# Kernel optimization log

Hardware: AMD Instinct MI355X
Metric: run time of the kernel (lower is better)

Reference implementation:

```python
import jax, jax.numpy as jnp
import numpy as np

TONECURVE_LENGTH = 256
RESOLUTION = 1024  # tone_curve_resolution
B, H, W = 8, 1024, 1536

RANGES = {
    'Temperature': (2000.0, 50000.0),
    'Tint': (-150.0, 150.0),
    'Exposure2012': (-5.0, 5.0),
    'Contrast2012': (-100.0, 100.0),
    'Highlights2012': (-100.0, 100.0),
    'Shadows2012': (-100.0, 100.0),
    'Whites2012': (-100.0, 100.0),
    'Blacks2012': (-100.0, 100.0),
    'Vibrance': (-100.0, 100.0),
    'Saturation': (-100.0, 100.0),
}

def _denorm(name, v):
    lo, hi = RANGES[name]
    return lo + 0.5 * (v + 1.0) * (hi - lo)

def _luminance(img):
    return 0.2126 * img[:, 0:1] + 0.7152 * img[:, 1:2] + 0.0722 * img[:, 2:3]

def _white_balance(img, temperature, tint):
    temp = jnp.clip(temperature, 2000.0, 50000.0)
    tr = 6500.0 / temp
    red = jnp.sqrt(tr)
    blue = 1.0 / jnp.sqrt(tr)
    ts = jnp.clip(tint / 150.0, -1.5, 1.5)
    green = 1.0 - 0.1 * ts
    red = red * (1.0 + 0.05 * ts)
    blue = blue * (1.0 - 0.05 * ts)
    gains = jnp.stack([red, green, blue], axis=1)[:, :, None, None]  # [B,3,1,1]
    balanced = img * gains
    norm = jnp.max(gains, axis=1, keepdims=True)
    return jnp.clip(balanced / jnp.maximum(norm, 1e-4), 0.0, 4.0)

def _region(img, luma, value, pivot, width):
    strength = (value / 100.0)[:, None, None, None]
    mask = jax.nn.sigmoid((luma - pivot) / width)
    mask = mask - jnp.mean(mask, axis=(2, 3), keepdims=True)
    new_luma = jnp.clip(luma + strength * mask, 0.0, 1.0)
    ratio = jnp.where(luma > 1e-4, new_luma / jnp.maximum(luma, 1e-4), 1.0)
    return jnp.clip(img * ratio, 0.0, 1.0), new_luma

def _tone_curve(img, tone_curve):
    luma = jnp.clip(_luminance(img), 0.0, 1.0)  # [B,1,H,W]
    # linear interp of [B,L] control points to [B,RESOLUTION], align_corners=True
    src = jnp.arange(RESOLUTION, dtype=jnp.float32) * ((TONECURVE_LENGTH - 1) / (RESOLUTION - 1))
    i0 = jnp.floor(src).astype(jnp.int32)
    i1 = jnp.minimum(i0 + 1, TONECURVE_LENGTH - 1)
    w = src - i0.astype(jnp.float32)
    curve = tone_curve[:, i0] * (1.0 - w) + tone_curve[:, i1] * w  # [B,RESOLUTION]
    coords = luma * (RESOLUTION - 1)
    idx_low = jnp.floor(coords).astype(jnp.int32)
    idx_high = jnp.minimum(idx_low + 1, RESOLUTION - 1)
    weight = coords - idx_low.astype(jnp.float32)
    b = img.shape[0]
    g_low = jnp.take_along_axis(curve, idx_low.reshape(b, -1), axis=1).reshape(luma.shape)
    g_high = jnp.take_along_axis(curve, idx_high.reshape(b, -1), axis=1).reshape(luma.shape)
    target = (1.0 - weight) * g_low + weight * g_high
    ratio = jnp.where(luma > 1e-5, target / jnp.maximum(luma, 1e-5), 1.0)
    return jnp.clip(img * ratio, 0.0, 1.0)

def _vibrance(img, vibrance):
    luma = _luminance(img)
    chroma = img - luma
    cn = jnp.sqrt(jnp.sum(chroma * chroma, axis=1, keepdims=True) + 1e-6)
    mask = jnp.exp(-4.0 * cn)
    gain = jnp.clip(1.0 + (vibrance / 100.0)[:, None, None, None] * mask, 0.2, 4.0)
    return jnp.clip(luma + chroma * gain, 0.0, 1.0)

def _saturation(img, saturation):
    luma = _luminance(img)
    chroma = img - luma
    gain = (1.0 + saturation / 100.0)[:, None, None, None]
    return jnp.clip(luma + chroma * gain, 0.0, 1.0)


def setup_inputs() -> dict:
    key = jax.random.key(0)
    ks = jax.random.split(key, 12)
    sliders = {}
    names = ['temperature_n', 'tint_n', 'exposure_n', 'contrast_n', 'highlights_n',
             'shadows_n', 'whites_n', 'blacks_n', 'vibrance_n', 'saturation_n']
    for i, n in enumerate(names):
        sliders[n] = jax.random.uniform(ks[i], (B,), jnp.float32, -1.0, 1.0)
    image = jax.random.uniform(ks[10], (B, 3, H, W), jnp.float32)
    tone_curve = jnp.sort(jax.random.uniform(ks[11], (B, TONECURVE_LENGTH), jnp.float32), axis=1)
    return {'image': image, 'tone_curve': tone_curve, **sliders}


def reference(image, tone_curve, temperature_n, tint_n, exposure_n, contrast_n,
              highlights_n, shadows_n, whites_n, blacks_n, vibrance_n, saturation_n):
    img = jnp.clip(image, 0.0, 1.0)
    temperature = _denorm('Temperature', temperature_n)
    tint = _denorm('Tint', tint_n)
    exposure = _denorm('Exposure2012', exposure_n)
    contrast = _denorm('Contrast2012', contrast_n)
    highlights = _denorm('Highlights2012', highlights_n)
    shadows = _denorm('Shadows2012', shadows_n)
    whites = _denorm('Whites2012', whites_n)
    blacks = _denorm('Blacks2012', blacks_n)
    vibrance = _denorm('Vibrance', vibrance_n)
    saturation = _denorm('Saturation', saturation_n)

    img = _white_balance(img, temperature, tint)
    img = img * jnp.power(2.0, exposure)[:, None, None, None]  # exposure
    img = jnp.clip(img, 0.0, 4.0)
    factor = (1.0 + contrast / 100.0)[:, None, None, None]      # contrast
    img = jnp.clip((img - 0.5) * factor + 0.5, 0.0, 1.0)

    luma = jnp.clip(_luminance(img), 0.0, 1.0)
    img, luma = _region(img, luma, highlights, 0.7, 0.1)
    img, luma = _region(img, luma, shadows, 0.3, 0.12)
    img, luma = _region(img, luma, whites, 0.9, 0.08)
    img, luma = _region(img, luma, blacks, 0.1, 0.08)

    img = _tone_curve(img, tone_curve)
    img = _vibrance(img, vibrance)
    img = _saturation(img, saturation)
    return jnp.clip(img, 0.0, 1.0)
```

## Files before the change

kernel.cpp:

```cpp
#include <hip/hip_runtime.h>
#include <math.h>

#define H_DIM 1024
#define W_DIM 1536
#define HW_PIX (H_DIM * W_DIM)
#define NBATCH 8
#define QPB (HW_PIX / 4)
#define BLKB 96
#define NBLK (NBATCH * BLKB)
#define QPT (QPB / (BLKB * 256))
#define RESOLUTION 1024
#define TC_LEN 256
#define SPIN_CAP 500000

typedef float vfloat4 __attribute__((ext_vector_type(4)));
typedef unsigned long long u64;

struct Sliders {
    const float* temperature; const float* tint; const float* exposure; const float* contrast;
    const float* highlights;  const float* shadows; const float* whites; const float* blacks;
    const float* vibrance;    const float* saturation;
};

__device__ __forceinline__ float denorm(float v, float lo, float hi) {
    return lo + 0.5f * (v + 1.0f) * (hi - lo);
}
__device__ __forceinline__ float clamp01(float x) {
    return __builtin_amdgcn_fmed3f(x, 0.f, 1.f);
}
__device__ __forceinline__ float clampf(float x, float lo, float hi) {
    return fminf(fmaxf(x, lo), hi);
}
__device__ __forceinline__ float sigmoidf(float x) {
    float t = __builtin_amdgcn_exp2f(x * -1.4426950408889634f);
    return __builtin_amdgcn_rcpf(1.0f + t);
}

struct FrontP { float sr, sg, sb, em, cf; };

__device__ __forceinline__ FrontP front_params(const Sliders& S, int b) {
    float temp = clampf(denorm(S.temperature[b], 2000.f, 50000.f), 2000.f, 50000.f);
    float tr   = 6500.f / temp;
    float red  = sqrtf(tr);
    float blue = 1.0f / sqrtf(tr);
    float ts   = clampf(denorm(S.tint[b], -150.f, 150.f) * (1.0f / 150.0f), -1.5f, 1.5f);
    float green = 1.0f - 0.1f * ts;
    red  *= (1.0f + 0.05f * ts);
    blue *= (1.0f - 0.05f * ts);
    float norm = fmaxf(fmaxf(red, green), blue);
    float inv  = 1.0f / fmaxf(norm, 1e-4f);
    FrontP p;
    p.sr = red * inv; p.sg = green * inv; p.sb = blue * inv;
    p.em = exp2f(denorm(S.exposure[b], -5.f, 5.f));
    p.cf = 1.0f + denorm(S.contrast[b], -100.f, 100.f) * 0.01f;
    return p;
}

__device__ __forceinline__ float front_chan(float x, float s, float em, float cf) {
    x = clamp01(x);
    x = x * s;
    x = fminf(x * em, 4.0f);
    return clamp01((x - 0.5f) * cf + 0.5f);
}

__device__ __forceinline__ float luminance(float r, float g, float b) {
    return 0.2126f * r + 0.7152f * g + 0.0722f * b;
}

__device__ __forceinline__ double block_sum_d(double v) {
    #pragma unroll
    for (int o = 32; o > 0; o >>= 1) v += __shfl_down(v, o, 64);
    __shared__ double s[4];
    int lane = threadIdx.x & 63, wid = threadIdx.x >> 6;
    if (lane == 0) s[wid] = v;
    __syncthreads();
    double r = 0.0;
    if (threadIdx.x == 0) r = s[0] + s[1] + s[2] + s[3];
    return r;
}

__device__ __forceinline__ void build_curve(float* curve, const float* tone_curve, int b) {
    const float* tc = tone_curve + b * TC_LEN;
    for (int j = threadIdx.x; j < RESOLUTION; j += 256) {
        float src = (float)j * ((float)(TC_LEN - 1) / (float)(RESOLUTION - 1));
        float fi  = floorf(src);
        int   i0  = (int)fi;
        int   i1  = min(i0 + 1, TC_LEN - 1);
        float w   = src - fi;
        curve[j]  = tc[i0] * (1.0f - w) + tc[i1] * w;
    }
}

__device__ __forceinline__ float publish_mean(int slot, int b, int bb, double acc,
                                              u64* part, unsigned int* meanc) {
    double tot = block_sum_d(acc);
    __shared__ float msh;
    const int pbase = (slot * NBATCH + b) * BLKB;
    const int tid = threadIdx.x;

    if (bb == 0) {
        double v = 0.0;
        if (tid == 0) v = tot;
        else if (tid < BLKB) {
            u64 x; int spins = 0;
            while ((x = __hip_atomic_load(&part[pbase + tid], __ATOMIC_RELAXED,
                                          __HIP_MEMORY_SCOPE_AGENT)) == 0ull) {
                __builtin_amdgcn_s_sleep(2);
                if (++spins > SPIN_CAP) break;
            }
            v = __builtin_bit_cast(double, x);
        }
        double t2 = block_sum_d(v);
        if (tid == 0) {
            float m = (float)(t2 * (1.0 / (double)HW_PIX));
            msh = m;
            __hip_atomic_store(&meanc[(slot * NBATCH + b) * 16],
                               __builtin_bit_cast(unsigned int, m),
                               __ATOMIC_RELAXED, __HIP_MEMORY_SCOPE_AGENT);
        }
    } else {
        if (tid == 0) {
            __hip_atomic_store(&part[pbase + bb], __builtin_bit_cast(u64, tot),
                               __ATOMIC_RELAXED, __HIP_MEMORY_SCOPE_AGENT);
            unsigned int x; int spins = 0;
            while ((x = __hip_atomic_load(&meanc[(slot * NBATCH + b) * 16],
                                          __ATOMIC_RELAXED,
                                          __HIP_MEMORY_SCOPE_AGENT)) == 0u) {
                __builtin_amdgcn_s_sleep(2);
                if (++spins > SPIN_CAP) break;
            }
            msh = __builtin_bit_cast(float, x);
        }
    }
    __syncthreads();
    float m = msh;
    __syncthreads();
    return m;
}

template <int K>
__device__ __forceinline__ double phaseB_acc(const unsigned short* __restrict__ lslice,
                                             int bb, int tid,
                                             const float* pivots, const float* invw,
                                             const float* strength, const float* meanv) {
    double acc = 0.0;
    for (int it = 0; it < QPT; it++) {
        const int off = (bb * (256 * QPT) + it * 256 + tid) * 4;
        ushort4 lq = *reinterpret_cast<const ushort4*>(lslice + off);
        const unsigned short* qs = reinterpret_cast<const unsigned short*>(&lq);
        #pragma unroll
        for (int i = 0; i < 4; i++) {
            float l = (float)qs[i] * (1.0f / 65535.0f);
            #pragma unroll
            for (int j = 0; j < K; j++) {
                float mask = sigmoidf((l - pivots[j]) * invw[j]);
                l = clamp01(l + strength[j] * (mask - meanv[j]));
            }
            acc += (double)sigmoidf((l - pivots[K]) * invw[K]);
        }
    }
    return acc;
}

__global__ __launch_bounds__(256, 4)
void mega_kernel(const float* __restrict__ image, const float* __restrict__ tone_curve,
                 Sliders S, unsigned int* __restrict__ meanc, u64* __restrict__ part,
                 unsigned short* __restrict__ ws_luma, float* __restrict__ out)
{
    const int b   = blockIdx.x / BLKB;
    const int bb  = blockIdx.x % BLKB;
    const int tid = threadIdx.x;

    __shared__ float curve[RESOLUTION];
    build_curve(curve, tone_curve, b);

    const float pivots[4] = {0.7f, 0.3f, 0.9f, 0.1f};
    const float invw[4]   = {1.0f / 0.1f, 1.0f / 0.12f, 1.0f / 0.08f, 1.0f / 0.08f};
    const float* sliders[4] = {S.highlights, S.shadows, S.whites, S.blacks};

    FrontP p = front_params(S, b);
    float strength[4];
    #pragma unroll
    for (int k = 0; k < 4; k++)
        strength[k] = denorm(sliders[k][b], -100.f, 100.f) * 0.01f;
    float vib  = denorm(S.vibrance[b],   -100.f, 100.f) * 0.01f;
    float satg = 1.0f + denorm(S.saturation[b], -100.f, 100.f) * 0.01f;

    unsigned short* lslice = ws_luma + (size_t)b * HW_PIX;
    const float* ibase = image + (size_t)b * 3 * HW_PIX;

    double acc = 0.0;
    for (int it = 0; it < QPT; it++) {
        const int off = (bb * (256 * QPT) + it * 256 + tid) * 4;
        float4 r4 = *reinterpret_cast<const float4*>(ibase + off);
        float4 g4 = *reinterpret_cast<const float4*>(ibase + HW_PIX + off);
        float4 b4 = *reinterpret_cast<const float4*>(ibase + 2 * HW_PIX + off);
        const float* rr  = reinterpret_cast<const float*>(&r4);
        const float* gg  = reinterpret_cast<const float*>(&g4);
        const float* bb4 = reinterpret_cast<const float*>(&b4);
        ushort4 pk;
        unsigned short* pks = reinterpret_cast<unsigned short*>(&pk);
        #pragma unroll
        for (int i = 0; i < 4; i++) {
            float r  = front_chan(rr[i],  p.sr, p.em, p.cf);
            float g  = front_chan(gg[i],  p.sg, p.em, p.cf);
            float bl = front_chan(bb4[i], p.sb, p.em, p.cf);
            float l  = clamp01(luminance(r, g, bl));
            acc += (double)sigmoidf((l - pivots[0]) * invw[0]);
            pks[i] = (unsigned short)(l * 65535.0f + 0.5f);
        }
        *reinterpret_cast<ushort4*>(lslice + off) = pk;
    }

    float meanv[4];
    meanv[0] = publish_mean(0, b, bb, acc, part, meanc);
    meanv[1] = publish_mean(1, b, bb,
                 phaseB_acc<1>(lslice, bb, tid, pivots, invw, strength, meanv), part, meanc);
    meanv[2] = publish_mean(2, b, bb,
                 phaseB_acc<2>(lslice, bb, tid, pivots, invw, strength, meanv), part, meanc);
    meanv[3] = publish_mean(3, b, bb,
                 phaseB_acc<3>(lslice, bb, tid, pivots, invw, strength, meanv), part, meanc);

    for (int it = 0; it < QPT; it++) {
        const int off = (bb * (256 * QPT) + it * 256 + tid) * 4;
        float4 r4 = *reinterpret_cast<const float4*>(ibase + off);
        float4 g4 = *reinterpret_cast<const float4*>(ibase + HW_PIX + off);
        float4 b4 = *reinterpret_cast<const float4*>(ibase + 2 * HW_PIX + off);
        float* rr  = reinterpret_cast<float*>(&r4);
        float* gg  = reinterpret_cast<float*>(&g4);
        float* bb4 = reinterpret_cast<float*>(&b4);

        #pragma unroll
        for (int i = 0; i < 4; i++) {
            float r  = front_chan(rr[i],  p.sr, p.em, p.cf);
            float g  = front_chan(gg[i],  p.sg, p.em, p.cf);
            float bl = front_chan(bb4[i], p.sb, p.em, p.cf);
            float lum = clamp01(luminance(r, g, bl));

            #pragma unroll
            for (int k = 0; k < 4; k++) {
                float mask = sigmoidf((lum - pivots[k]) * invw[k]);
                float nl   = clamp01(lum + strength[k] * (mask - meanv[k]));
                float ratio = (lum > 1e-4f) ? nl * __builtin_amdgcn_rcpf(lum) : 1.0f;
                r  = fminf(r * ratio, 1.f);
                g  = fminf(g * ratio, 1.f);
                bl = fminf(bl * ratio, 1.f);
                lum = nl;
            }

            float tl = clamp01(luminance(r, g, bl));
            float coords = tl * (float)(RESOLUTION - 1);
            float fidx = floorf(coords);
            int   i0 = (int)fidx;
            int   i1 = min(i0 + 1, RESOLUTION - 1);
            float w  = coords - fidx;
            float target = (1.0f - w) * curve[i0] + w * curve[i1];
            float ratio  = (tl > 1e-5f) ? target * __builtin_amdgcn_rcpf(tl) : 1.0f;
            r  = fminf(r * ratio, 1.f);
            g  = fminf(g * ratio, 1.f);
            bl = fminf(bl * ratio, 1.f);

            float l2 = luminance(r, g, bl);
            float cr = r - l2, cg = g - l2, cb = bl - l2;
            float cn = sqrtf(cr * cr + cg * cg + cb * cb + 1e-6f);
            float gmask = __builtin_amdgcn_exp2f(cn * -5.771f);
            float vg = __builtin_amdgcn_fmed3f(1.0f + vib * gmask, 0.2f, 4.0f);
            r  = clamp01(l2 + cr * vg);
            g  = clamp01(l2 + cg * vg);
            bl = clamp01(l2 + cb * vg);

            float l3 = luminance(r, g, bl);
            r  = clamp01(l3 + (r - l3) * satg);
            g  = clamp01(l3 + (g - l3) * satg);
            bl = clamp01(l3 + (bl - l3) * satg);

            rr[i] = r; gg[i] = g; bb4[i] = bl;
        }

        float* op = out + (size_t)b * 3 * HW_PIX + off;
        __builtin_nontemporal_store(*reinterpret_cast<vfloat4*>(&r4),
                                    reinterpret_cast<vfloat4*>(op));
        __builtin_nontemporal_store(*reinterpret_cast<vfloat4*>(&g4),
                                    reinterpret_cast<vfloat4*>(op + HW_PIX));
        __builtin_nontemporal_store(*reinterpret_cast<vfloat4*>(&b4),
                                    reinterpret_cast<vfloat4*>(op + 2 * HW_PIX));
    }
}

extern "C" void kernel_launch(void* const* d_in, const int* in_sizes, int n_in,
                              void* d_out, int out_size, void* d_ws, size_t ws_size,
                              hipStream_t stream) {
    const float* image      = (const float*)d_in[0];
    const float* tone_curve = (const float*)d_in[1];
    Sliders S;
    S.temperature = (const float*)d_in[2];
    S.tint        = (const float*)d_in[3];
    S.exposure    = (const float*)d_in[4];
    S.contrast    = (const float*)d_in[5];
    S.highlights  = (const float*)d_in[6];
    S.shadows     = (const float*)d_in[7];
    S.whites      = (const float*)d_in[8];
    S.blacks      = (const float*)d_in[9];
    S.vibrance    = (const float*)d_in[10];
    S.saturation  = (const float*)d_in[11];
    float* out = (float*)d_out;

    unsigned int*   meanc   = (unsigned int*)d_ws;
    u64*            part    = (u64*)((char*)d_ws + 2048);
    unsigned short* ws_luma = (unsigned short*)((char*)d_ws + 32768);

    hipMemsetAsync(d_ws, 0, 2048 + 4 * NBATCH * BLKB * sizeof(u64), stream);

    mega_kernel<<<dim3(NBLK), dim3(256), 0, stream>>>(image, tone_curve, S,
                                                      meanc, part, ws_luma, out);
}
```

Measured before the change: 386.5 us.

## Keep per-pixel luma in registers across reduction phases instead of global workspace

```diff
diff --git a/kernel.cpp b/kernel.cpp
--- a/kernel.cpp
+++ b/kernel.cpp
@@ -6,9 +6,10 @@
 #define HW_PIX (H_DIM * W_DIM)
 #define NBATCH 8
 #define QPB (HW_PIX / 4)
-#define BLKB 96
+#define BLKB 128
 #define NBLK (NBATCH * BLKB)
 #define QPT (QPB / (BLKB * 256))
+#define NLUM (QPT * 4)
 #define RESOLUTION 1024
 #define TC_LEN 256
 #define SPIN_CAP 500000
@@ -138,34 +139,10 @@
     return m;
 }
 
-template <int K>
-__device__ __forceinline__ double phaseB_acc(const unsigned short* __restrict__ lslice,
-                                             int bb, int tid,
-                                             const float* pivots, const float* invw,
-                                             const float* strength, const float* meanv) {
-    double acc = 0.0;
-    for (int it = 0; it < QPT; it++) {
-        const int off = (bb * (256 * QPT) + it * 256 + tid) * 4;
-        ushort4 lq = *reinterpret_cast<const ushort4*>(lslice + off);
-        const unsigned short* qs = reinterpret_cast<const unsigned short*>(&lq);
-        #pragma unroll
-        for (int i = 0; i < 4; i++) {
-            float l = (float)qs[i] * (1.0f / 65535.0f);
-            #pragma unroll
-            for (int j = 0; j < K; j++) {
-                float mask = sigmoidf((l - pivots[j]) * invw[j]);
-                l = clamp01(l + strength[j] * (mask - meanv[j]));
-            }
-            acc += (double)sigmoidf((l - pivots[K]) * invw[K]);
-        }
-    }
-    return acc;
-}
-
 __global__ __launch_bounds__(256, 4)
 void mega_kernel(const float* __restrict__ image, const float* __restrict__ tone_curve,
                  Sliders S, unsigned int* __restrict__ meanc, u64* __restrict__ part,
-                 unsigned short* __restrict__ ws_luma, float* __restrict__ out)
+                 float* __restrict__ out)
 {
     const int b   = blockIdx.x / BLKB;
     const int bb  = blockIdx.x % BLKB;
@@ -186,10 +163,11 @@
     float vib  = denorm(S.vibrance[b],   -100.f, 100.f) * 0.01f;
     float satg = 1.0f + denorm(S.saturation[b], -100.f, 100.f) * 0.01f;
 
-    unsigned short* lslice = ws_luma + (size_t)b * HW_PIX;
     const float* ibase = image + (size_t)b * 3 * HW_PIX;
 
+    float lum[NLUM];
     double acc = 0.0;
+    #pragma unroll
     for (int it = 0; it < QPT; it++) {
         const int off = (bb * (256 * QPT) + it * 256 + tid) * 4;
         float4 r4 = *reinterpret_cast<const float4*>(ibase + off);
@@ -198,28 +176,33 @@
         const float* rr  = reinterpret_cast<const float*>(&r4);
         const float* gg  = reinterpret_cast<const float*>(&g4);
         const float* bb4 = reinterpret_cast<const float*>(&b4);
-        ushort4 pk;
-        unsigned short* pks = reinterpret_cast<unsigned short*>(&pk);
         #pragma unroll
         for (int i = 0; i < 4; i++) {
             float r  = front_chan(rr[i],  p.sr, p.em, p.cf);
             float g  = front_chan(gg[i],  p.sg, p.em, p.cf);
             float bl = front_chan(bb4[i], p.sb, p.em, p.cf);
             float l  = clamp01(luminance(r, g, bl));
+            lum[it * 4 + i] = l;
             acc += (double)sigmoidf((l - pivots[0]) * invw[0]);
-            pks[i] = (unsigned short)(l * 65535.0f + 0.5f);
-        }
-        *reinterpret_cast<ushort4*>(lslice + off) = pk;
+        }
     }
 
     float meanv[4];
-    meanv[0] = publish_mean(0, b, bb, acc, part, meanc);
-    meanv[1] = publish_mean(1, b, bb,
-                 phaseB_acc<1>(lslice, bb, tid, pivots, invw, strength, meanv), part, meanc);
-    meanv[2] = publish_mean(2, b, bb,
-                 phaseB_acc<2>(lslice, bb, tid, pivots, invw, strength, meanv), part, meanc);
-    meanv[3] = publish_mean(3, b, bb,
-                 phaseB_acc<3>(lslice, bb, tid, pivots, invw, strength, meanv), part, meanc);
+    #pragma unroll
+    for (int k = 0; k < 4; k++) {
+        meanv[k] = publish_mean(k, b, bb, acc, part, meanc);
+        if (k < 3) {
+            acc = 0.0;
+            #pragma unroll
+            for (int j = 0; j < NLUM; j++) {
+                float l    = lum[j];
+                float mask = sigmoidf((l - pivots[k]) * invw[k]);
+                l = clamp01(l + strength[k] * (mask - meanv[k]));
+                lum[j] = l;
+                acc += (double)sigmoidf((l - pivots[k + 1]) * invw[k + 1]);
+            }
+        }
+    }
 
     for (int it = 0; it < QPT; it++) {
         const int off = (bb * (256 * QPT) + it * 256 + tid) * 4;
@@ -235,17 +218,17 @@
             float r  = front_chan(rr[i],  p.sr, p.em, p.cf);
             float g  = front_chan(gg[i],  p.sg, p.em, p.cf);
             float bl = front_chan(bb4[i], p.sb, p.em, p.cf);
-            float lum = clamp01(luminance(r, g, bl));
+            float lm = clamp01(luminance(r, g, bl));
 
             #pragma unroll
             for (int k = 0; k < 4; k++) {
-                float mask = sigmoidf((lum - pivots[k]) * invw[k]);
-                float nl   = clamp01(lum + strength[k] * (mask - meanv[k]));
-                float ratio = (lum > 1e-4f) ? nl * __builtin_amdgcn_rcpf(lum) : 1.0f;
+                float mask = sigmoidf((lm - pivots[k]) * invw[k]);
+                float nl   = clamp01(lm + strength[k] * (mask - meanv[k]));
+                float ratio = (lm > 1e-4f) ? nl * __builtin_amdgcn_rcpf(lm) : 1.0f;
                 r  = fminf(r * ratio, 1.f);
                 g  = fminf(g * ratio, 1.f);
                 bl = fminf(bl * ratio, 1.f);
-                lum = nl;
+                lm = nl;
             }
 
             float tl = clamp01(luminance(r, g, bl));
@@ -305,12 +288,11 @@
     S.saturation  = (const float*)d_in[11];
     float* out = (float*)d_out;
 
-    unsigned int*   meanc   = (unsigned int*)d_ws;
-    u64*            part    = (u64*)((char*)d_ws + 2048);
-    unsigned short* ws_luma = (unsigned short*)((char*)d_ws + 32768);
+    unsigned int* meanc = (unsigned int*)d_ws;
+    u64*          part  = (u64*)((char*)d_ws + 2048);
 
     hipMemsetAsync(d_ws, 0, 2048 + 4 * NBATCH * BLKB * sizeof(u64), stream);
 
     mega_kernel<<<dim3(NBLK), dim3(256), 0, stream>>>(image, tone_curve, S,
-                                                      meanc, part, ws_luma, out);
-}
+                                                      meanc, part, out);
+}
```

New measurement: 328.4 us. 1.18x faster.
